# Optimization experiments

Measured on AMD Instinct MI355X. Metric: run time of the kernel, lower is better.

Reference implementation:

```python
import jax, jax.numpy as jnp
import numpy as np

H = 16  # hidden_size
I = 30  # GRU input_size (hard-coded in module)


def setup_inputs() -> dict:
    key = jax.random.key(0)
    ks = jax.random.split(key, 12)
    B, T = 4096, 512
    s = lambda k, sh: jax.random.normal(k, sh, jnp.float32) * 0.1
    return {
        "x": jax.random.normal(ks[0], (B, T, I), jnp.float32),
        "lengths": jax.random.randint(ks[1], (B,), 1, T + 1),  # valid lengths in [1, T]
        "w_ih": s(ks[2], (3 * H, I)),
        "w_hh": s(ks[3], (3 * H, H)),
        "b_ih": s(ks[4], (3 * H,)),
        "b_hh": s(ks[5], (3 * H,)),
        "fc1_w": s(ks[6], (H, H)), "fc1_b": s(ks[7], (H,)),
        "fc2_w": s(ks[8], (H, H)), "fc2_b": s(ks[9], (H,)),
        "fc3_w": s(ks[10], (H, H)), "fc3_b": s(ks[11], (H,)),
    }


def _gru_last_hidden(x, lengths, w_ih, w_hh, b_ih, b_hh):
    """Run GRU over padded [B,T,I] and return hidden at t = lengths-1 per row.
    Equivalent to pack_padded -> GRU -> pad_packed -> gather output[b, len-1],
    since h_t only depends on steps <= t."""
    B, T, _ = x.shape
    # Precompute input-side gate activations for all steps: [B,T,3H]
    xg = jnp.einsum('bti,gi->btg', x, w_ih) + b_ih
    xr, xz, xn = jnp.split(xg, 3, axis=-1)
    w_hr, w_hz, w_hn = jnp.split(w_hh, 3, axis=0)
    b_hr, b_hz, b_hn = jnp.split(b_hh, 3)
    tidx = lengths - 1  # [B]

    def step(carry, inp):
        h, last = carry
        t, xr_t, xz_t, xn_t = inp
        r = jax.nn.sigmoid(xr_t + h @ w_hr.T + b_hr)
        z = jax.nn.sigmoid(xz_t + h @ w_hz.T + b_hz)
        n = jnp.tanh(xn_t + r * (h @ w_hn.T + b_hn))
        h = (1.0 - z) * n + z * h
        last = jnp.where((tidx == t)[:, None], h, last)  # capture h at final valid step
        return (h, last), None

    h0 = jnp.zeros((B, H), x.dtype)
    (_, last), _ = jax.lax.scan(
        step, (h0, h0),
        (jnp.arange(T),
         xr.transpose(1, 0, 2), xz.transpose(1, 0, 2), xn.transpose(1, 0, 2)))
    return last  # [B,H]


def reference(x, lengths, w_ih, w_hh, b_ih, b_hh,
              fc1_w, fc1_b, fc2_w, fc2_b, fc3_w, fc3_b):
    h = _gru_last_hidden(x, lengths, w_ih, w_hh, b_ih, b_hh)
    e = h @ fc1_w.T + fc1_b
    e = jax.nn.relu(e) @ fc2_w.T + fc2_b   # dropout is identity in eval mode
    e = jax.nn.relu(e) @ fc3_w.T + fc3_b
    return e
```

## Files before the change

kernel.cpp:

```cpp
#include <hip/hip_runtime.h>
#include <cstdint>
#include <cstddef>

typedef float v2f __attribute__((ext_vector_type(2)));

#define HID 16
#define IN  30

#define FAST_RCP(x) __builtin_amdgcn_rcpf(x)

__device__ __forceinline__ float fsig(float x) {
    float e = __expf(-x);
    return FAST_RCP(1.0f + e);
}
__device__ __forceinline__ float ftanh(float x) {
    float e = __expf(2.0f * x);
    return fmaf(-2.0f, FAST_RCP(e + 1.0f), 1.0f);
}
__device__ __forceinline__ float bperm(int baddr, float v) {
    return __int_as_float(__builtin_amdgcn_ds_bpermute(baddr, __float_as_int(v)));
}
__device__ __forceinline__ float dppswap1(float v) {
    return __int_as_float(__builtin_amdgcn_mov_dpp(__float_as_int(v), 0xB1, 0xF, 0xF, true));
}
#define PKFMA(acc, a, b) asm("v_pk_fma_f32 %0, %1, %2, %0" : "+v"(acc) : "v"(a), "v"(b))

__global__ void k_hist(const int* __restrict__ len, int* __restrict__ hist, int B, int T) {
    int i = blockIdx.x * 256 + threadIdx.x;
    if (i < B) atomicAdd(hist + (T - len[i]), 1);
}
__global__ __launch_bounds__(512) void k_scan(const int* __restrict__ hist, int* __restrict__ off) {
    __shared__ int s[512];
    int t = threadIdx.x;
    int v = hist[t];
    s[t] = v; __syncthreads();
    int acc = v;
    for (int o = 1; o < 512; o <<= 1) {
        int add = (t >= o) ? s[t - o] : 0;
        __syncthreads();
        acc += add; s[t] = acc;
        __syncthreads();
    }
    off[t] = acc - v;
}
__global__ void k_scatter(const int* __restrict__ len, int* __restrict__ off,
                          int* __restrict__ perm, int B, int T) {
    int i = blockIdx.x * 256 + threadIdx.x;
    if (i < B) {
        int b = T - len[i];
        int p = atomicAdd(off + b, 1);
        perm[p] = i;
    }
}

__global__ __launch_bounds__(512, 2) void gru_enc_kernel(
    const float* __restrict__ x, const int* __restrict__ lengths,
    const float* __restrict__ w_ih, const float* __restrict__ w_hh,
    const float* __restrict__ b_ih, const float* __restrict__ b_hh,
    const float* __restrict__ fc1w, const float* __restrict__ fc1b,
    const float* __restrict__ fc2w, const float* __restrict__ fc2b,
    const float* __restrict__ fc3w, const float* __restrict__ fc3b,
    float* __restrict__ out, const int* __restrict__ perm,
    int B, int T, int NP, int nblk)
{
    const int lane = threadIdx.x & 63;
    const int wib  = threadIdx.x >> 6;
    const int rb   = lane & 32;
    const int half = lane & 1;
    const int j    = (lane >> 1) & 15;

    int pos;
    if (wib < 4) pos = 4 * blockIdx.x + wib;
    else         pos = NP - 1 - (4 * blockIdx.x + (wib - 4));
    if (pos < 0 || pos >= NP) return;
    if (wib >= 4 && pos < 4 * nblk) return;

    int ridx = 2 * pos + (rb >> 5);
    if (ridx >= B) ridx = B - 1;
    const int row = perm ? perm[ridx] : ridx;

    const int len = lengths[row];
    const int maxlen = max(len, __shfl_xor(len, 32));

    v2f wih2[3][8];
#pragma unroll
    for (int g = 0; g < 3; ++g) {
        const float* wr = w_ih + (size_t)(g * HID + j) * IN;
#pragma unroll
        for (int m = 0; m < 8; ++m) {
            int p0 = 2 * m, p1 = 2 * m + 1;
            v2f t;
            if (half) { t.x = (p0 == 0) ? 0.0f : wr[14 + p0]; t.y = wr[14 + p1]; }
            else      { t.x = wr[p0]; t.y = (p1 == 15) ? 0.0f : wr[p1]; }
            wih2[g][m] = t;
        }
    }
    v2f whh2[3][4];
#pragma unroll
    for (int g = 0; g < 3; ++g)
#pragma unroll
        for (int m = 0; m < 4; ++m) {
            const float* wr = w_hh + (size_t)(g * HID + j) * HID + half * 8 + 2 * m;
            v2f t; t.x = wr[0]; t.y = wr[1];
            whh2[g][m] = t;
        }

    v2f initR; initR.x = half ? 0.0f : (b_ih[j] + b_hh[j]);               initR.y = 0.0f;
    v2f initZ; initZ.x = half ? 0.0f : (b_ih[HID + j] + b_hh[HID + j]);   initZ.y = 0.0f;
    v2f initN; initN.x = half ? 0.0f : b_ih[2 * HID + j];                 initN.y = 0.0f;
    v2f initH; initH.x = half ? 0.0f : b_hh[2 * HID + j];                 initH.y = 0.0f;

    const float* xr = x + (size_t)row * T * IN + (half ? 14 : 0);

    int ba0[4], ba1[4];
#pragma unroll
    for (int m = 0; m < 4; ++m) {
        int k0 = half * 8 + 2 * m;
        ba0[m] = (rb | (k0 << 1)) << 2;
        ba1[m] = (rb | ((k0 + 1) << 1)) << 2;
    }

#define LOADX(buf, tt) do {                                        \
        const v2f* p_ = (const v2f*)(xr + (size_t)(tt) * IN);      \
        _Pragma("unroll")                                          \
        for (int m_ = 0; m_ < 8; ++m_) buf[m_] = p_[m_];           \
    } while (0)

#define STEP(t, xv) do {                                                    \
        v2f ar = initR, az = initZ, an = initN, hn = initH;                 \
        _Pragma("unroll")                                                   \
        for (int m_ = 0; m_ < 8; ++m_) {                                    \
            PKFMA(ar, wih2[0][m_], xv[m_]);                                 \
            PKFMA(az, wih2[1][m_], xv[m_]);                                 \
            PKFMA(an, wih2[2][m_], xv[m_]);                                 \
        }                                                                   \
        _Pragma("unroll")                                                   \
        for (int m_ = 0; m_ < 4; ++m_) {                                    \
            PKFMA(ar, whh2[0][m_], hb2[m_]);                                \
            PKFMA(az, whh2[1][m_], hb2[m_]);                                \
            PKFMA(hn, whh2[2][m_], hb2[m_]);                                \
        }                                                                   \
        float pr  = ar.x + ar.y;  pr  += dppswap1(pr);                      \
        float pz  = az.x + az.y;  pz  += dppswap1(pz);                      \
        float pxn = an.x + an.y;  pxn += dppswap1(pxn);                     \
        float phn = hn.x + hn.y;  phn += dppswap1(phn);                     \
        float rg = fsig(pr);                                                \
        float zg = fsig(pz);                                                \
        float ng = ftanh(fmaf(rg, phn, pxn));                               \
        float hnew = fmaf(zg, h_own - ng, ng);                              \
        last  = ((t) == len - 1) ? hnew : last;                             \
        h_own = hnew;                                                       \
        _Pragma("unroll")                                                   \
        for (int m_ = 0; m_ < 4; ++m_) {                                    \
            hb2[m_].x = bperm(ba0[m_], hnew);                               \
            hb2[m_].y = bperm(ba1[m_], hnew);                               \
        }                                                                   \
    } while (0)

    v2f hb2[4];
#pragma unroll
    for (int m = 0; m < 4; ++m) { hb2[m].x = 0.0f; hb2[m].y = 0.0f; }
    float h_own = 0.0f, last = 0.0f;

    v2f xa[8], xb[8];
    LOADX(xa, 0);
    LOADX(xb, (T > 1) ? 1 : 0);

    const int tcap = T - 1;
    for (int t = 0; t < maxlen; t += 2) {
        STEP(t, xa);
        LOADX(xa, min(t + 2, tcap));
        STEP(t + 1, xb);
        LOADX(xb, min(t + 3, tcap));
    }

    float hv[16];
#pragma unroll
    for (int k = 0; k < 16; ++k) hv[k] = __shfl(last, rb + 2 * k, 64);

    float e1 = fc1b[j];
#pragma unroll
    for (int k = 0; k < 16; ++k) e1 = fmaf(fc1w[j * HID + k], hv[k], e1);

    float v1[16];
#pragma unroll
    for (int k = 0; k < 16; ++k) v1[k] = fmaxf(__shfl(e1, rb + 2 * k, 64), 0.0f);

    float e2 = fc2b[j];
#pragma unroll
    for (int k = 0; k < 16; ++k) e2 = fmaf(fc2w[j * HID + k], v1[k], e2);

    float v2a[16];
#pragma unroll
    for (int k = 0; k < 16; ++k) v2a[k] = fmaxf(__shfl(e2, rb + 2 * k, 64), 0.0f);

    float e3 = fc3b[j];
#pragma unroll
    for (int k = 0; k < 16; ++k) e3 = fmaf(fc3w[j * HID + k], v2a[k], e3);

    if (half == 0) out[(size_t)row * HID + j] = e3;
}

extern "C" void kernel_launch(void* const* d_in, const int* in_sizes, int n_in,
                              void* d_out, int out_size, void* d_ws, size_t ws_size,
                              hipStream_t stream) {
    const float* x    = (const float*)d_in[0];
    const int*   lens = (const int*)d_in[1];
    const float* w_ih = (const float*)d_in[2];
    const float* w_hh = (const float*)d_in[3];
    const float* b_ih = (const float*)d_in[4];
    const float* b_hh = (const float*)d_in[5];
    const float* fc1w = (const float*)d_in[6];
    const float* fc1b = (const float*)d_in[7];
    const float* fc2w = (const float*)d_in[8];
    const float* fc2b = (const float*)d_in[9];
    const float* fc3w = (const float*)d_in[10];
    const float* fc3b = (const float*)d_in[11];
    float* out = (float*)d_out;

    const int B = in_sizes[1];
    const int T = (int)(in_sizes[0] / ((size_t)B * IN));

    int* wsI = (int*)d_ws;
    const size_t need = ((size_t)B + 1024) * sizeof(int);
    const bool dosort = (ws_size >= need) && (T <= 512) && (T >= 1);
    int* perm = dosort ? wsI : nullptr;
    int* hist = wsI + B;
    int* off  = wsI + B + 512;

    if (dosort) {
        hipMemsetAsync(hist, 0, 512 * sizeof(int), stream);
        k_hist<<<(B + 255) / 256, 256, 0, stream>>>(lens, hist, B, T);
        k_scan<<<1, 512, 0, stream>>>(hist, off);
        k_scatter<<<(B + 255) / 256, 256, 0, stream>>>(lens, off, perm, B, T);
    }

    const int NP   = (B + 1) / 2;
    const int nblk = (NP + 7) / 8;
    gru_enc_kernel<<<nblk, 512, 0, stream>>>(x, lens, w_ih, w_hh, b_ih, b_hh,
                                             fc1w, fc1b, fc2w, fc2b, fc3w, fc3b,
                                             out, perm, B, T, NP, nblk);
}
```

Baseline: 156.6 us.

## Stage x through LDS with async global_load_lds ring buffer and exp2 gates

Replaces direct per-step register loads of the input sequence with a 4-deep LDS ring buffer filled by asynchronous global_load_lds in 8-timestep chunks, issued three chunks ahead and throttled by s_waitcnt vmcnt. Each lane loads one of 30 features, which gives coalesced row loads, and the step reads its 16 floats from LDS. The gate weights and biases are also pre-scaled by ±log2(e) so sigmoid and tanh can use exp2 directly, which removes a multiply per activation. The cost is 64KB of LDS per block, which may limit occupancy. The hard-coded vmcnt count and the missing barrier before LDS reads are risky; the sort threshold also changes to T>=8.

```diff
diff --git a/kernel.cpp b/kernel.cpp
--- a/kernel.cpp
+++ b/kernel.cpp
@@ -9,14 +9,6 @@
 
 #define FAST_RCP(x) __builtin_amdgcn_rcpf(x)
 
-__device__ __forceinline__ float fsig(float x) {
-    float e = __expf(-x);
-    return FAST_RCP(1.0f + e);
-}
-__device__ __forceinline__ float ftanh(float x) {
-    float e = __expf(2.0f * x);
-    return fmaf(-2.0f, FAST_RCP(e + 1.0f), 1.0f);
-}
 __device__ __forceinline__ float bperm(int baddr, float v) {
     return __int_as_float(__builtin_amdgcn_ds_bpermute(baddr, __float_as_int(v)));
 }
@@ -24,6 +16,11 @@
     return __int_as_float(__builtin_amdgcn_mov_dpp(__float_as_int(v), 0xB1, 0xF, 0xF, true));
 }
 #define PKFMA(acc, a, b) asm("v_pk_fma_f32 %0, %1, %2, %0" : "+v"(acc) : "v"(a), "v"(b))
+
+typedef __attribute__((address_space(3))) unsigned int       lds_u32_t;
+typedef const __attribute__((address_space(1))) unsigned int glb_u32_t;
+#define GLOAD_LDS(gp, lp) \
+    __builtin_amdgcn_global_load_lds((glb_u32_t*)(gp), (lds_u32_t*)(lp), 4, 0, 0)
 
 __global__ void k_hist(const int* __restrict__ len, int* __restrict__ hist, int B, int T) {
     int i = blockIdx.x * 256 + threadIdx.x;
@@ -63,6 +60,8 @@
     float* __restrict__ out, const int* __restrict__ perm,
     int B, int T, int NP, int nblk)
 {
+    __shared__ __align__(16) float lds[8][4][8][64];
+
     const int lane = threadIdx.x & 63;
     const int wib  = threadIdx.x >> 6;
     const int rb   = lane & 32;
@@ -82,6 +81,10 @@
     const int len = lengths[row];
     const int maxlen = max(len, __shfl_xor(len, 32));
 
+    const float L2E = 1.4426950408889634f;
+
+    const float gsc[3] = { -L2E, -L2E, 2.0f * L2E };
+
     v2f wih2[3][8];
 #pragma unroll
     for (int g = 0; g < 3; ++g) {
@@ -92,6 +95,7 @@
             v2f t;
             if (half) { t.x = (p0 == 0) ? 0.0f : wr[14 + p0]; t.y = wr[14 + p1]; }
             else      { t.x = wr[p0]; t.y = (p1 == 15) ? 0.0f : wr[p1]; }
+            t.x *= gsc[g]; t.y *= gsc[g];
             wih2[g][m] = t;
         }
     }
@@ -101,16 +105,20 @@
 #pragma unroll
         for (int m = 0; m < 4; ++m) {
             const float* wr = w_hh + (size_t)(g * HID + j) * HID + half * 8 + 2 * m;
-            v2f t; t.x = wr[0]; t.y = wr[1];
+            v2f t; t.x = wr[0] * gsc[g]; t.y = wr[1] * gsc[g];
             whh2[g][m] = t;
         }
 
-    v2f initR; initR.x = half ? 0.0f : (b_ih[j] + b_hh[j]);               initR.y = 0.0f;
-    v2f initZ; initZ.x = half ? 0.0f : (b_ih[HID + j] + b_hh[HID + j]);   initZ.y = 0.0f;
-    v2f initN; initN.x = half ? 0.0f : b_ih[2 * HID + j];                 initN.y = 0.0f;
-    v2f initH; initH.x = half ? 0.0f : b_hh[2 * HID + j];                 initH.y = 0.0f;
-
-    const float* xr = x + (size_t)row * T * IN + (half ? 14 : 0);
+    v2f initR; initR.x = half ? 0.0f : -L2E * (b_ih[j] + b_hh[j]);                 initR.y = 0.0f;
+    v2f initZ; initZ.x = half ? 0.0f : -L2E * (b_ih[HID + j] + b_hh[HID + j]);     initZ.y = 0.0f;
+    v2f initN; initN.x = half ? 0.0f : 2.0f * L2E * b_ih[2 * HID + j];             initN.y = 0.0f;
+    v2f initH; initH.x = half ? 0.0f : 2.0f * L2E * b_hh[2 * HID + j];             initH.y = 0.0f;
+
+    const int kk = min(lane & 31, 29);
+    const float* xg = x + (size_t)row * T * IN + kk;
+
+    float* ldsw = &lds[wib][0][0][0];
+    const float* ldsr = ldsw + (rb ? 32 : 0) + half * 14;
 
     int ba0[4], ba1[4];
 #pragma unroll
@@ -120,14 +128,24 @@
         ba1[m] = (rb | ((k0 + 1) << 1)) << 2;
     }
 
-#define LOADX(buf, tt) do {                                        \
-        const v2f* p_ = (const v2f*)(xr + (size_t)(tt) * IN);      \
-        _Pragma("unroll")                                          \
-        for (int m_ = 0; m_ < 8; ++m_) buf[m_] = p_[m_];           \
+    const int tcap = T - 1;
+
+#define STAGE(cc) do {                                                     \
+        const int t0_ = (cc) << 3;                                         \
+        float* lb_ = ldsw + (((cc) & 3) << 9);                             \
+        _Pragma("unroll")                                                  \
+        for (int s_ = 0; s_ < 8; ++s_) {                                   \
+            int ts_ = min(t0_ + s_, tcap);                                 \
+            GLOAD_LDS(xg + (size_t)ts_ * IN, lb_ + (s_ << 6));             \
+        }                                                                  \
     } while (0)
 
-#define STEP(t, xv) do {                                                    \
+#define STEP(t, cw, s) do {                                                 \
         v2f ar = initR, az = initZ, an = initN, hn = initH;                 \
+        v2f xv[8];                                                          \
+        _Pragma("unroll")                                                   \
+        for (int m_ = 0; m_ < 8; ++m_)                                      \
+            xv[m_] = *(const v2f*)((cw) + ((s) << 6) + (m_ << 1));          \
         _Pragma("unroll")                                                   \
         for (int m_ = 0; m_ < 8; ++m_) {                                    \
             PKFMA(ar, wih2[0][m_], xv[m_]);                                 \
@@ -144,9 +162,10 @@
         float pz  = az.x + az.y;  pz  += dppswap1(pz);                      \
         float pxn = an.x + an.y;  pxn += dppswap1(pxn);                     \
         float phn = hn.x + hn.y;  phn += dppswap1(phn);                     \
-        float rg = fsig(pr);                                                \
-        float zg = fsig(pz);                                                \
-        float ng = ftanh(fmaf(rg, phn, pxn));                               \
+        float rg = FAST_RCP(1.0f + __builtin_exp2f(pr));                    \
+        float zg = FAST_RCP(1.0f + __builtin_exp2f(pz));                    \
+        float yy = fmaf(rg, phn, pxn);                                      \
+        float ng = fmaf(-2.0f, FAST_RCP(1.0f + __builtin_exp2f(yy)), 1.0f); \
         float hnew = fmaf(zg, h_own - ng, ng);                              \
         last  = ((t) == len - 1) ? hnew : last;                             \
         h_own = hnew;                                                       \
@@ -162,16 +181,21 @@
     for (int m = 0; m < 4; ++m) { hb2[m].x = 0.0f; hb2[m].y = 0.0f; }
     float h_own = 0.0f, last = 0.0f;
 
-    v2f xa[8], xb[8];
-    LOADX(xa, 0);
-    LOADX(xb, (T > 1) ? 1 : 0);
-
-    const int tcap = T - 1;
-    for (int t = 0; t < maxlen; t += 2) {
-        STEP(t, xa);
-        LOADX(xa, min(t + 2, tcap));
-        STEP(t + 1, xb);
-        LOADX(xb, min(t + 3, tcap));
+    const int nch = (maxlen + 7) >> 3;
+
+    STAGE(0); STAGE(1); STAGE(2);
+
+    for (int c = 0; c < nch; ++c) {
+        asm volatile("s_waitcnt vmcnt(16)" ::: "memory");
+        STAGE(c + 3);
+        const float* cw = ldsr + ((c & 3) << 9);
+        const int nst = min(8, maxlen - (c << 3));
+        const int tb = c << 3;
+#pragma unroll
+        for (int s = 0; s < 8; ++s) {
+            if (s >= nst) break;
+            STEP(tb + s, cw, s);
+        }
     }
 
     float hv[16];
@@ -223,7 +247,7 @@
 
     int* wsI = (int*)d_ws;
     const size_t need = ((size_t)B + 1024) * sizeof(int);
-    const bool dosort = (ws_size >= need) && (T <= 512) && (T >= 1);
+    const bool dosort = (ws_size >= need) && (T <= 512) && (T >= 8);
     int* perm = dosort ? wsI : nullptr;
     int* hist = wsI + B;
     int* off  = wsI + B + 512;
```

After: 171.4 us. +9.5%, slower.
